# Kernel optimization log

Hardware: AMD Instinct MI355X
Metric: run time of the kernel (lower is better)

## Reference

```python
import jax, jax.numpy as jnp
import numpy as np

B, N, E, DJ, DE = 1024, 400, 128, 128, 128  # batch, nodes, edges, joint dim, edge dim (E must equal DJ and DE for BatchNorm1d on 3D input)
BN_EPS = 1e-5


def setup_inputs() -> dict:
    key = jax.random.key(0)
    ks = jax.random.split(key, 8)
    gout = jax.random.normal(ks[0], (B, N, DJ), dtype=jnp.float32)
    eout = jax.random.normal(ks[1], (B, E, DE), dtype=jnp.float32)
    start_shift = jax.random.uniform(ks[2], (B, E, N), dtype=jnp.float32)
    end_shift = jax.random.uniform(ks[3], (B, E, N), dtype=jnp.float32)
    # Linear params: nn.init.normal_(std=0.001), bias 0
    W1 = 0.001 * jax.random.normal(ks[4], (DJ, 2 * DJ), dtype=jnp.float32)
    b1 = jnp.zeros((DJ,), dtype=jnp.float32)
    W2 = 0.001 * jax.random.normal(ks[5], (DE, DJ), dtype=jnp.float32)
    b2 = jnp.zeros((DE,), dtype=jnp.float32)
    # BatchNorm affine params: weight=1, bias=0
    g1 = jnp.ones((DJ,), dtype=jnp.float32)
    beta1 = jnp.zeros((DJ,), dtype=jnp.float32)
    g2 = jnp.ones((DE,), dtype=jnp.float32)
    beta2 = jnp.zeros((DE,), dtype=jnp.float32)
    return {"gout": gout, "eout": eout, "start_shift": start_shift, "end_shift": end_shift,
            "W1": W1, "b1": b1, "W2": W2, "b2": b2,
            "g1": g1, "beta1": beta1, "g2": g2, "beta2": beta2}


def batchnorm1d(x, gamma, beta):
    # PyTorch BatchNorm1d on 3D input: channels at dim 1, biased variance over dims (0, 2)
    mean = jnp.mean(x, axis=(0, 2), keepdims=True)
    var = jnp.mean(jnp.square(x - mean), axis=(0, 2), keepdims=True)
    xhat = (x - mean) * jax.lax.rsqrt(var + BN_EPS)
    return xhat * gamma[None, :, None] + beta[None, :, None]


def reference(gout, eout, start_shift, end_shift, W1, b1, W2, b2, g1, beta1, g2, beta2):
    # node -> edge gather via dense shift matmuls: [B,E,N] @ [B,N,DJ] -> [B,E,DJ]
    start_nodes = jnp.matmul(start_shift, gout)
    end_nodes = jnp.matmul(end_shift, gout)
    x = jnp.concatenate([start_nodes, end_nodes], axis=2)  # [B, E, 2*DJ]
    h = jnp.einsum('bef,df->bed', x, W1) + b1  # Linear(2*DJ -> DJ)
    h = jax.nn.relu(batchnorm1d(h, g1, beta1))
    h = jnp.einsum('bed,od->beo', h, W2) + b2  # Linear(DJ -> DE)
    res = batchnorm1d(h, g2, beta2)
    return jax.nn.relu(eout + res)
```

## Files before the change

kernel.cpp:

```cpp
#include <hip/hip_runtime.h>
#include <stdint.h>

#define BB 1024
#define NN 400
#define EE 128
#define DD 128
#define NSLOT 64

typedef float f32x4 __attribute__((ext_vector_type(4)));
typedef float f32x2 __attribute__((ext_vector_type(2)));
typedef short bf16x8 __attribute__((ext_vector_type(8)));
typedef short bf16x4 __attribute__((ext_vector_type(4)));

__device__ __forceinline__ short f2bf(float f) {
    uint32_t u = __builtin_bit_cast(uint32_t, f);
    u += 0x7fffu + ((u >> 16) & 1u);
    return (short)(u >> 16);
}

__device__ __forceinline__ float bf2f(short s) {
    return __builtin_bit_cast(float, (uint32_t)((uint16_t)s) << 16);
}

__device__ __forceinline__ bf16x8 cvt8(const f32x4 a, const f32x4 b) {
    bf16x8 r;
    r[0] = f2bf(a[0]); r[1] = f2bf(a[1]); r[2] = f2bf(a[2]); r[3] = f2bf(a[3]);
    r[4] = f2bf(b[0]); r[5] = f2bf(b[1]); r[6] = f2bf(b[2]); r[7] = f2bf(b[3]);
    return r;
}

__global__ __launch_bounds__(256, 4)
void k1_gemm(const float* __restrict__ gout, const float* __restrict__ ss,
             const float* __restrict__ es, const float* __restrict__ W1,
             const float* __restrict__ b1, unsigned short* __restrict__ h,
             float* __restrict__ stats1)
{
    __shared__ short lds[16384];
    short* As = lds;
    short* Gs = lds + 5120;
    short* Ps = lds;

    const int bid = blockIdx.x;
    const int b   = bid >> 1;
    const int e0  = (bid & 1) * 64;
    const int t   = threadIdx.x;
    const int w   = t >> 6;
    const int l15 = t & 15;
    const int l4  = (t >> 4) & 3;

    f32x4 acc[2][8];
#pragma unroll
    for (int i = 0; i < 2; ++i)
#pragma unroll
        for (int j = 0; j < 8; ++j) acc[i][j] = f32x4{0.f, 0.f, 0.f, 0.f};

    f32x4 ar[4];
    const int arow = t >> 3;
    const int acol = (t & 7) * 4;
    f32x2 g0[4], g1[4];
    const int gx = t & 31;
    const int gk = (t >> 5) * 2;

    auto load_a = [&](int k0) {
#pragma unroll
        for (int p = 0; p < 4; ++p) {
            int row = arow + 32 * p;
            int col = k0 + acol;
            const float* src = (row < 64)
                ? ss + (size_t)(b * EE + e0 + row) * NN + col
                : es + (size_t)(b * EE + e0 + row - 64) * NN + col;
            ar[p] = (col < NN) ? *(const f32x4*)src : f32x4{0.f, 0.f, 0.f, 0.f};
        }
    };
    auto load_g = [&](int k0) {
#pragma unroll
        for (int p = 0; p < 4; ++p) {
            int d0 = 2 * gx + 64 * (p & 1);
            int k  = k0 + gk + 16 * (p >> 1);
            const float* base = gout + (size_t)b * NN * DD + (size_t)k * DD + d0;
            g0[p] = (k < NN)     ? *(const f32x2*)base        : f32x2{0.f, 0.f};
            g1[p] = (k + 1 < NN) ? *(const f32x2*)(base + DD) : f32x2{0.f, 0.f};
        }
    };
    auto store_a = [&]() {
#pragma unroll
        for (int p = 0; p < 4; ++p) {
            int row = arow + 32 * p;
            bf16x4 v;
            v[0] = f2bf(ar[p][0]); v[1] = f2bf(ar[p][1]);
            v[2] = f2bf(ar[p][2]); v[3] = f2bf(ar[p][3]);
            *(bf16x4*)&As[row * 40 + acol] = v;
        }
    };
    auto store_g = [&]() {
#pragma unroll
        for (int p = 0; p < 4; ++p) {
            int d0 = 2 * gx + 64 * (p & 1);
            int kp = gk + 16 * (p >> 1);
            uint32_t lo = (uint32_t)(uint16_t)f2bf(g0[p][0]) |
                          ((uint32_t)(uint16_t)f2bf(g1[p][0]) << 16);
            uint32_t hi = (uint32_t)(uint16_t)f2bf(g0[p][1]) |
                          ((uint32_t)(uint16_t)f2bf(g1[p][1]) << 16);
            int c  = (kp >> 3) ^ ((d0 >> 2) & 3);
            int a0 = d0 * 40 + (c << 3) + (kp & 7);
            *(uint32_t*)&Gs[a0]      = lo;
            *(uint32_t*)&Gs[a0 + 40] = hi;
        }
    };

    load_a(0); load_g(0);
    const int NK = (NN + 31) / 32;
    for (int step = 0; step < NK; ++step) {
        store_a(); store_g();
        __syncthreads();
        if (step + 1 < NK) { load_a((step + 1) * 32); load_g((step + 1) * 32); }
        bf16x8 af[2];
#pragma unroll
        for (int rf = 0; rf < 2; ++rf) {
            int row = w * 32 + rf * 16 + l15;
            af[rf] = *(const bf16x8*)&As[row * 40 + l4 * 8];
        }
#pragma unroll
        for (int cf = 0; cf < 8; ++cf) {
            int col = cf * 16 + l15;
            int cc  = l4 ^ ((col >> 2) & 3);
            bf16x8 bfr = *(const bf16x8*)&Gs[col * 40 + cc * 8];
            acc[0][cf] = __builtin_amdgcn_mfma_f32_16x16x32_bf16(af[0], bfr, acc[0][cf], 0, 0, 0);
            acc[1][cf] = __builtin_amdgcn_mfma_f32_16x16x32_bf16(af[1], bfr, acc[1][cf], 0, 0, 0);
        }
        __syncthreads();
    }

#pragma unroll
    for (int rf = 0; rf < 2; ++rf)
#pragma unroll
        for (int cf = 0; cf < 8; ++cf)
#pragma unroll
            for (int r = 0; r < 4; ++r) {
                int row = w * 32 + rf * 16 + l4 * 4 + r;
                int col = cf * 16 + l15;
                int off = row * 128 + (((col >> 3) ^ (row & 7)) * 8) + (col & 7);
                Ps[off] = f2bf(acc[rf][cf][r]);
            }
    __syncthreads();

    f32x4 hacc[4][2];
#pragma unroll
    for (int i = 0; i < 4; ++i) {
        hacc[i][0] = f32x4{0.f, 0.f, 0.f, 0.f};
        hacc[i][1] = f32x4{0.f, 0.f, 0.f, 0.f};
    }
#pragma unroll
    for (int kf = 0; kf < 8; ++kf) {
        const int k0   = kf * 32;
        const int roff = (kf >= 4) ? 64 : 0;
        const int cb   = ((k0 & 127) >> 3) + l4;
        bf16x8 af[4];
#pragma unroll
        for (int rf = 0; rf < 4; ++rf) {
            int row = roff + rf * 16 + l15;
            af[rf] = *(const bf16x8*)&Ps[row * 128 + ((cb ^ (row & 7)) * 8)];
        }
#pragma unroll
        for (int cf = 0; cf < 2; ++cf) {
            int j = w * 32 + cf * 16 + l15;
            const float* wp = W1 + (size_t)j * 256 + k0 + l4 * 8;
            bf16x8 bfr = cvt8(*(const f32x4*)wp, *(const f32x4*)(wp + 4));
#pragma unroll
            for (int rf = 0; rf < 4; ++rf)
                hacc[rf][cf] = __builtin_amdgcn_mfma_f32_16x16x32_bf16(af[rf], bfr, hacc[rf][cf], 0, 0, 0);
        }
    }
    __syncthreads();

    float* red = (float*)lds;
    const float bj0 = b1[w * 32 + l15];
    const float bj1 = b1[w * 32 + 16 + l15];
    const int j0 = w * 32 + l15;
#pragma unroll
    for (int rf = 0; rf < 4; ++rf) {
        f32x4 v0 = hacc[rf][0] + bj0;
        f32x4 v1 = hacc[rf][1] + bj1;
        int elb = rf * 16 + l4 * 4;
#pragma unroll
        for (int r = 0; r < 4; ++r) {
            unsigned short* hp = h + (size_t)(b * EE + e0 + elb + r) * DD;
            hp[j0]      = (unsigned short)f2bf(v0[r]);
            hp[j0 + 16] = (unsigned short)f2bf(v1[r]);
            float s = v0[r] + v1[r];
            float q = v0[r] * v0[r] + v1[r] * v1[r];
            s += __shfl_xor(s, 1); s += __shfl_xor(s, 2); s += __shfl_xor(s, 4); s += __shfl_xor(s, 8);
            q += __shfl_xor(q, 1); q += __shfl_xor(q, 2); q += __shfl_xor(q, 4); q += __shfl_xor(q, 8);
            if (l15 == 0) {
                red[(elb + r) * 4 + w]       = s;
                red[256 + (elb + r) * 4 + w] = q;
            }
        }
    }
    __syncthreads();
    if (t < 64) {
        float s = red[t * 4] + red[t * 4 + 1] + red[t * 4 + 2] + red[t * 4 + 3];
        float q = red[256 + t * 4] + red[256 + t * 4 + 1] + red[256 + t * 4 + 2] + red[256 + t * 4 + 3];
        int slot = bid & (NSLOT - 1);
        atomicAdd(&stats1[slot * 256 + e0 + t], s);
        atomicAdd(&stats1[slot * 256 + 128 + e0 + t], q);
    }
}

__global__ __launch_bounds__(256, 4)
void k3_gemm(const unsigned short* __restrict__ h, const float* __restrict__ W2,
             const float* __restrict__ b2, const float* __restrict__ g1,
             const float* __restrict__ bt1, float* __restrict__ out,
             const float* __restrict__ stats1, float* __restrict__ stats2)
{
    __shared__ short Xs[128 * 128];
    __shared__ float sc[128];
    __shared__ float sh[128];
    const int b   = blockIdx.x;
    const int t   = threadIdx.x;
    const int w   = t >> 6;
    const int l15 = t & 15;
    const int l4  = (t >> 4) & 3;

    if (t < 128) {
        float sm = 0.f, sq = 0.f;
#pragma unroll 8
        for (int sl = 0; sl < NSLOT; ++sl) {
            sm += stats1[sl * 256 + t];
            sq += stats1[sl * 256 + 128 + t];
        }
        const float inv_n = 1.0f / (1024.0f * 128.0f);
        float m    = sm * inv_n;
        float var  = sq * inv_n - m * m;
        float rstd = rsqrtf(var + 1e-5f);
        float s    = rstd * g1[t];
        sc[t] = s;
        sh[t] = bt1[t] - m * s;
    }
    __syncthreads();

    {
        const int c8 = t & 15;
        const int eb = t >> 4;
#pragma unroll
        for (int p = 0; p < 8; ++p) {
            int e = eb + 16 * p;
            bf16x8 v8 = *(const bf16x8*)&h[((size_t)b * EE + e) * DD + c8 * 8];
            float s = sc[e], s0 = sh[e];
            bf16x8 o;
#pragma unroll
            for (int i = 0; i < 8; ++i)
                o[i] = f2bf(fmaxf(fmaf(bf2f(v8[i]), s, s0), 0.0f));
            *(bf16x8*)&Xs[e * 128 + ((c8 ^ (e & 7)) << 3)] = o;
        }
    }
    __syncthreads();

    f32x4 acc[8][2];
#pragma unroll
    for (int i = 0; i < 8; ++i) {
        acc[i][0] = f32x4{0.f, 0.f, 0.f, 0.f};
        acc[i][1] = f32x4{0.f, 0.f, 0.f, 0.f};
    }
#pragma unroll
    for (int kf = 0; kf < 4; ++kf) {
        const int k0 = kf * 32;
        const int cb = (k0 >> 3) + l4;
        bf16x8 af[8];
#pragma unroll
        for (int rf = 0; rf < 8; ++rf) {
            int row = rf * 16 + l15;
            af[rf] = *(const bf16x8*)&Xs[row * 128 + ((cb ^ (row & 7)) * 8)];
        }
#pragma unroll
        for (int cf = 0; cf < 2; ++cf) {
            int j = w * 32 + cf * 16 + l15;
            const float* wp = W2 + (size_t)j * 128 + k0 + l4 * 8;
            bf16x8 bfr = cvt8(*(const f32x4*)wp, *(const f32x4*)(wp + 4));
#pragma unroll
            for (int rf = 0; rf < 8; ++rf)
                acc[rf][cf] = __builtin_amdgcn_mfma_f32_16x16x32_bf16(af[rf], bfr, acc[rf][cf], 0, 0, 0);
        }
    }

    __syncthreads();
    float* red = (float*)Xs;
    const float bj0 = b2[w * 32 + l15];
    const float bj1 = b2[w * 32 + 16 + l15];
    const int j0 = w * 32 + l15;
#pragma unroll
    for (int rf = 0; rf < 8; ++rf) {
        f32x4 v0 = acc[rf][0] + bj0;
        f32x4 v1 = acc[rf][1] + bj1;
        int elb = rf * 16 + l4 * 4;
#pragma unroll
        for (int r = 0; r < 4; ++r) {
            float* op = out + (size_t)(b * EE + elb + r) * DD;
            op[j0]      = v0[r];
            op[j0 + 16] = v1[r];
            float s = v0[r] + v1[r];
            float q = v0[r] * v0[r] + v1[r] * v1[r];
            s += __shfl_xor(s, 1); s += __shfl_xor(s, 2); s += __shfl_xor(s, 4); s += __shfl_xor(s, 8);
            q += __shfl_xor(q, 1); q += __shfl_xor(q, 2); q += __shfl_xor(q, 4); q += __shfl_xor(q, 8);
            if (l15 == 0) {
                red[(elb + r) * 4 + w]       = s;
                red[512 + (elb + r) * 4 + w] = q;
            }
        }
    }
    __syncthreads();
    if (t < 128) {
        float s = red[t * 4] + red[t * 4 + 1] + red[t * 4 + 2] + red[t * 4 + 3];
        float q = red[512 + t * 4] + red[512 + t * 4 + 1] + red[512 + t * 4 + 2] + red[512 + t * 4 + 3];
        int slot = b & (NSLOT - 1);
        atomicAdd(&stats2[slot * 256 + t], s);
        atomicAdd(&stats2[slot * 256 + 128 + t], q);
    }
}

__global__ __launch_bounds__(256)
void k5_final(const float* __restrict__ eout, const float* __restrict__ g2,
              const float* __restrict__ bt2, float* __restrict__ io,
              const float* __restrict__ stats2)
{
    __shared__ float sc[128];
    __shared__ float sh[128];
    const int t = threadIdx.x;
    if (t < 128) {
        float sm = 0.f, sq = 0.f;
#pragma unroll 8
        for (int sl = 0; sl < NSLOT; ++sl) {
            sm += stats2[sl * 256 + t];
            sq += stats2[sl * 256 + 128 + t];
        }
        const float inv_n = 1.0f / (1024.0f * 128.0f);
        float m    = sm * inv_n;
        float var  = sq * inv_n - m * m;
        float rstd = rsqrtf(var + 1e-5f);
        float s    = rstd * g2[t];
        sc[t] = s;
        sh[t] = bt2[t] - m * s;
    }
    __syncthreads();

    const int total4 = BB * EE * DD / 4;
    for (int i4 = blockIdx.x * blockDim.x + t; i4 < total4; i4 += gridDim.x * blockDim.x) {
        int e = (i4 >> 5) & 127;
        f32x4 v = *(f32x4*)(io + (size_t)i4 * 4);
        f32x4 u = *(const f32x4*)(eout + (size_t)i4 * 4);
        float s = sc[e], s0 = sh[e];
        f32x4 o;
#pragma unroll
        for (int i = 0; i < 4; ++i)
            o[i] = fmaxf(u[i] + fmaf(v[i], s, s0), 0.0f);
        *(f32x4*)(io + (size_t)i4 * 4) = o;
    }
}

extern "C" void kernel_launch(void* const* d_in, const int* in_sizes, int n_in,
                              void* d_out, int out_size, void* d_ws, size_t ws_size,
                              hipStream_t stream)
{
    const float* gout  = (const float*)d_in[0];
    const float* eout  = (const float*)d_in[1];
    const float* ss    = (const float*)d_in[2];
    const float* es    = (const float*)d_in[3];
    const float* W1    = (const float*)d_in[4];
    const float* b1    = (const float*)d_in[5];
    const float* W2    = (const float*)d_in[6];
    const float* b2    = (const float*)d_in[7];
    const float* g1    = (const float*)d_in[8];
    const float* bt1   = (const float*)d_in[9];
    const float* g2    = (const float*)d_in[10];
    const float* bt2   = (const float*)d_in[11];

    float* stats1 = (float*)d_ws;
    float* stats2 = stats1 + NSLOT * 256;
    unsigned short* h = (unsigned short*)(stats2 + NSLOT * 256);
    float* out    = (float*)d_out;

    hipMemsetAsync((void*)stats1, 0, 2 * NSLOT * 256 * sizeof(float), stream);
    k1_gemm<<<dim3(BB * 2), dim3(256), 0, stream>>>(gout, ss, es, W1, b1, h, stats1);
    k3_gemm<<<dim3(BB), dim3(256), 0, stream>>>(h, W2, b2, g1, bt1, out, stats1, stats2);
    k5_final<<<dim3(2048), dim3(256), 0, stream>>>(eout, g2, bt2, out, stats2);
}
```

Baseline: 258.0 us.

## Restructure k1 to one 1024-thread block per batch with full gout staged in LDS

The first GEMM kernel now runs one 1024-thread block per batch instead of two 256-thread blocks. The whole transposed gout tile is converted to bf16 once into LDS, so it is no longer loaded twice per batch. Shift-matrix rows stream straight from global memory into MFMA A fragments, with register prefetch in place of LDS staging and per-step barriers. W1 is staged in LDS as bf16 for the second GEMM instead of being re-read from global by every wave. The cost is about 133KB of LDS per block, which allows only one block per CU, and the shift-matrix global loads are less coalesced.

```diff
diff --git a/kernel.cpp b/kernel.cpp
--- a/kernel.cpp
+++ b/kernel.cpp
@@ -6,9 +6,10 @@
 #define EE 128
 #define DD 128
 #define NSLOT 64
+#define GTS 424
+#define NKP 212
 
 typedef float f32x4 __attribute__((ext_vector_type(4)));
-typedef float f32x2 __attribute__((ext_vector_type(2)));
 typedef short bf16x8 __attribute__((ext_vector_type(8)));
 typedef short bf16x4 __attribute__((ext_vector_type(4)));
 
@@ -29,181 +30,145 @@
     return r;
 }
 
-__global__ __launch_bounds__(256, 4)
+__global__ __launch_bounds__(1024, 1)
 void k1_gemm(const float* __restrict__ gout, const float* __restrict__ ss,
              const float* __restrict__ es, const float* __restrict__ W1,
              const float* __restrict__ b1, unsigned short* __restrict__ h,
              float* __restrict__ stats1)
 {
-    __shared__ short lds[16384];
-    short* As = lds;
-    short* Gs = lds + 5120;
-    short* Ps = lds;
-
-    const int bid = blockIdx.x;
-    const int b   = bid >> 1;
-    const int e0  = (bid & 1) * 64;
+    __shared__ short lds[66560];
+    short* GT  = lds;
+    short* Ps  = lds;
+    short* W1s = lds + 32768;
+
+    const int b   = blockIdx.x;
     const int t   = threadIdx.x;
     const int w   = t >> 6;
-    const int l15 = t & 15;
-    const int l4  = (t >> 4) & 3;
-
-    f32x4 acc[2][8];
-#pragma unroll
-    for (int i = 0; i < 2; ++i)
-#pragma unroll
-        for (int j = 0; j < 8; ++j) acc[i][j] = f32x4{0.f, 0.f, 0.f, 0.f};
-
-    f32x4 ar[4];
-    const int arow = t >> 3;
-    const int acol = (t & 7) * 4;
-    f32x2 g0[4], g1[4];
-    const int gx = t & 31;
-    const int gk = (t >> 5) * 2;
-
-    auto load_a = [&](int k0) {
-#pragma unroll
-        for (int p = 0; p < 4; ++p) {
-            int row = arow + 32 * p;
-            int col = k0 + acol;
-            const float* src = (row < 64)
-                ? ss + (size_t)(b * EE + e0 + row) * NN + col
-                : es + (size_t)(b * EE + e0 + row - 64) * NN + col;
-            ar[p] = (col < NN) ? *(const f32x4*)src : f32x4{0.f, 0.f, 0.f, 0.f};
-        }
+    const int l   = t & 63;
+    const int l15 = l & 15;
+    const int l4  = l >> 4;
+
+    {
+        const int d   = t & 127;
+        const int kpb = t >> 7;
+        const float* gb = gout + (size_t)b * NN * DD + d;
+        for (int kp = kpb; kp < NKP; kp += 8) {
+            int k = 2 * kp;
+            float v0 = 0.f, v1 = 0.f;
+            if (k < NN) { v0 = gb[(size_t)k * DD]; v1 = gb[(size_t)(k + 1) * DD]; }
+            uint32_t pk = (uint32_t)(uint16_t)f2bf(v0) |
+                          ((uint32_t)(uint16_t)f2bf(v1) << 16);
+            *(uint32_t*)&GT[d * GTS + 2 * kp] = pk;
+        }
+    }
+    __syncthreads();
+
+    const int arow = (w & 7) * 16 + l15;
+    const float* abase = ((w < 8) ? ss : es) + ((size_t)b * EE + arow) * NN;
+
+    f32x4 acc[8];
+#pragma unroll
+    for (int cf = 0; cf < 8; ++cf) acc[cf] = f32x4{0.f, 0.f, 0.f, 0.f};
+
+    auto ld_a = [&](int k0) -> bf16x8 {
+        int kk = k0 + l4 * 8;
+        f32x4 x0{0.f, 0.f, 0.f, 0.f}, x1{0.f, 0.f, 0.f, 0.f};
+        if (kk < NN) { x0 = *(const f32x4*)(abase + kk); x1 = *(const f32x4*)(abase + kk + 4); }
+        return cvt8(x0, x1);
     };
-    auto load_g = [&](int k0) {
-#pragma unroll
-        for (int p = 0; p < 4; ++p) {
-            int d0 = 2 * gx + 64 * (p & 1);
-            int k  = k0 + gk + 16 * (p >> 1);
-            const float* base = gout + (size_t)b * NN * DD + (size_t)k * DD + d0;
-            g0[p] = (k < NN)     ? *(const f32x2*)base        : f32x2{0.f, 0.f};
-            g1[p] = (k + 1 < NN) ? *(const f32x2*)(base + DD) : f32x2{0.f, 0.f};
-        }
-    };
-    auto store_a = [&]() {
-#pragma unroll
-        for (int p = 0; p < 4; ++p) {
-            int row = arow + 32 * p;
-            bf16x4 v;
-            v[0] = f2bf(ar[p][0]); v[1] = f2bf(ar[p][1]);
-            v[2] = f2bf(ar[p][2]); v[3] = f2bf(ar[p][3]);
-            *(bf16x4*)&As[row * 40 + acol] = v;
-        }
-    };
-    auto store_g = [&]() {
-#pragma unroll
-        for (int p = 0; p < 4; ++p) {
-            int d0 = 2 * gx + 64 * (p & 1);
-            int kp = gk + 16 * (p >> 1);
-            uint32_t lo = (uint32_t)(uint16_t)f2bf(g0[p][0]) |
-                          ((uint32_t)(uint16_t)f2bf(g1[p][0]) << 16);
-            uint32_t hi = (uint32_t)(uint16_t)f2bf(g0[p][1]) |
-                          ((uint32_t)(uint16_t)f2bf(g1[p][1]) << 16);
-            int c  = (kp >> 3) ^ ((d0 >> 2) & 3);
-            int a0 = d0 * 40 + (c << 3) + (kp & 7);
-            *(uint32_t*)&Gs[a0]      = lo;
-            *(uint32_t*)&Gs[a0 + 40] = hi;
-        }
-    };
-
-    load_a(0); load_g(0);
-    const int NK = (NN + 31) / 32;
-    for (int step = 0; step < NK; ++step) {
-        store_a(); store_g();
-        __syncthreads();
-        if (step + 1 < NK) { load_a((step + 1) * 32); load_g((step + 1) * 32); }
-        bf16x8 af[2];
-#pragma unroll
-        for (int rf = 0; rf < 2; ++rf) {
-            int row = w * 32 + rf * 16 + l15;
-            af[rf] = *(const bf16x8*)&As[row * 40 + l4 * 8];
-        }
+
+    bf16x8 a_cur = ld_a(0);
+    const int NK = 13;
+    for (int s = 0; s < NK; ++s) {
+        bf16x8 a_nxt = a_cur;
+        if (s + 1 < NK) a_nxt = ld_a((s + 1) * 32);
+        const int k0 = s * 32;
 #pragma unroll
         for (int cf = 0; cf < 8; ++cf) {
+            bf16x8 gf = *(const bf16x8*)&GT[(cf * 16 + l15) * GTS + k0 + l4 * 8];
+            acc[cf] = __builtin_amdgcn_mfma_f32_16x16x32_bf16(a_cur, gf, acc[cf], 0, 0, 0);
+        }
+        a_cur = a_nxt;
+    }
+    __syncthreads();
+
+#pragma unroll
+    for (int cf = 0; cf < 8; ++cf)
+#pragma unroll
+        for (int r = 0; r < 4; ++r) {
+            int row = w * 16 + l4 * 4 + r;
             int col = cf * 16 + l15;
-            int cc  = l4 ^ ((col >> 2) & 3);
-            bf16x8 bfr = *(const bf16x8*)&Gs[col * 40 + cc * 8];
-            acc[0][cf] = __builtin_amdgcn_mfma_f32_16x16x32_bf16(af[0], bfr, acc[0][cf], 0, 0, 0);
-            acc[1][cf] = __builtin_amdgcn_mfma_f32_16x16x32_bf16(af[1], bfr, acc[1][cf], 0, 0, 0);
-        }
-        __syncthreads();
-    }
-
-#pragma unroll
-    for (int rf = 0; rf < 2; ++rf)
-#pragma unroll
-        for (int cf = 0; cf < 8; ++cf)
-#pragma unroll
-            for (int r = 0; r < 4; ++r) {
-                int row = w * 32 + rf * 16 + l4 * 4 + r;
-                int col = cf * 16 + l15;
-                int off = row * 128 + (((col >> 3) ^ (row & 7)) * 8) + (col & 7);
-                Ps[off] = f2bf(acc[rf][cf][r]);
-            }
-    __syncthreads();
-
-    f32x4 hacc[4][2];
-#pragma unroll
-    for (int i = 0; i < 4; ++i) {
-        hacc[i][0] = f32x4{0.f, 0.f, 0.f, 0.f};
-        hacc[i][1] = f32x4{0.f, 0.f, 0.f, 0.f};
-    }
+            Ps[row * 128 + (((col >> 3) ^ (row & 7)) << 3) + (col & 7)] = f2bf(acc[cf][r]);
+        }
+    {
+        const int j  = t >> 3;
+        const int kc = t & 7;
+        const float* wp = W1 + (size_t)j * 256 + kc * 32;
+        short* dst = &W1s[j * 264 + kc * 32];
+#pragma unroll
+        for (int i = 0; i < 4; ++i) {
+            f32x4 x0 = *(const f32x4*)(wp + i * 8);
+            f32x4 x1 = *(const f32x4*)(wp + i * 8 + 4);
+            *(bf16x8*)(dst + i * 8) = cvt8(x0, x1);
+        }
+    }
+    __syncthreads();
+
+    const int mt = w >> 1;
+    const int jh = w & 1;
+    f32x4 acc2[4];
+#pragma unroll
+    for (int cf = 0; cf < 4; ++cf) acc2[cf] = f32x4{0.f, 0.f, 0.f, 0.f};
+
 #pragma unroll
     for (int kf = 0; kf < 8; ++kf) {
-        const int k0   = kf * 32;
-        const int roff = (kf >= 4) ? 64 : 0;
-        const int cb   = ((k0 & 127) >> 3) + l4;
-        bf16x8 af[4];
-#pragma unroll
-        for (int rf = 0; rf < 4; ++rf) {
-            int row = roff + rf * 16 + l15;
-            af[rf] = *(const bf16x8*)&Ps[row * 128 + ((cb ^ (row & 7)) * 8)];
-        }
-#pragma unroll
-        for (int cf = 0; cf < 2; ++cf) {
-            int j = w * 32 + cf * 16 + l15;
-            const float* wp = W1 + (size_t)j * 256 + k0 + l4 * 8;
-            bf16x8 bfr = cvt8(*(const f32x4*)wp, *(const f32x4*)(wp + 4));
-#pragma unroll
-            for (int rf = 0; rf < 4; ++rf)
-                hacc[rf][cf] = __builtin_amdgcn_mfma_f32_16x16x32_bf16(af[rf], bfr, hacc[rf][cf], 0, 0, 0);
+        int roff = (kf >= 4) ? 128 : 0;
+        int kcol = (kf & 3) * 32 + l4 * 8;
+        int row  = roff + mt * 16 + l15;
+        int cb   = kcol >> 3;
+        bf16x8 xf = *(const bf16x8*)&Ps[row * 128 + ((cb ^ (row & 7)) << 3)];
+#pragma unroll
+        for (int cf = 0; cf < 4; ++cf) {
+            int j = jh * 64 + cf * 16 + l15;
+            bf16x8 wf = *(const bf16x8*)&W1s[j * 264 + kf * 32 + l4 * 8];
+            acc2[cf] = __builtin_amdgcn_mfma_f32_16x16x32_bf16(xf, wf, acc2[cf], 0, 0, 0);
         }
     }
     __syncthreads();
 
     float* red = (float*)lds;
-    const float bj0 = b1[w * 32 + l15];
-    const float bj1 = b1[w * 32 + 16 + l15];
-    const int j0 = w * 32 + l15;
-#pragma unroll
-    for (int rf = 0; rf < 4; ++rf) {
-        f32x4 v0 = hacc[rf][0] + bj0;
-        f32x4 v1 = hacc[rf][1] + bj1;
-        int elb = rf * 16 + l4 * 4;
+    float s_r[4] = {0.f, 0.f, 0.f, 0.f};
+    float q_r[4] = {0.f, 0.f, 0.f, 0.f};
+#pragma unroll
+    for (int cf = 0; cf < 4; ++cf) {
+        float bv = b1[jh * 64 + cf * 16 + l15];
+        f32x4 v = acc2[cf] + bv;
 #pragma unroll
         for (int r = 0; r < 4; ++r) {
-            unsigned short* hp = h + (size_t)(b * EE + e0 + elb + r) * DD;
-            hp[j0]      = (unsigned short)f2bf(v0[r]);
-            hp[j0 + 16] = (unsigned short)f2bf(v1[r]);
-            float s = v0[r] + v1[r];
-            float q = v0[r] * v0[r] + v1[r] * v1[r];
-            s += __shfl_xor(s, 1); s += __shfl_xor(s, 2); s += __shfl_xor(s, 4); s += __shfl_xor(s, 8);
-            q += __shfl_xor(q, 1); q += __shfl_xor(q, 2); q += __shfl_xor(q, 4); q += __shfl_xor(q, 8);
-            if (l15 == 0) {
-                red[(elb + r) * 4 + w]       = s;
-                red[256 + (elb + r) * 4 + w] = q;
-            }
-        }
-    }
-    __syncthreads();
-    if (t < 64) {
-        float s = red[t * 4] + red[t * 4 + 1] + red[t * 4 + 2] + red[t * 4 + 3];
-        float q = red[256 + t * 4] + red[256 + t * 4 + 1] + red[256 + t * 4 + 2] + red[256 + t * 4 + 3];
-        int slot = bid & (NSLOT - 1);
-        atomicAdd(&stats1[slot * 256 + e0 + t], s);
-        atomicAdd(&stats1[slot * 256 + 128 + e0 + t], q);
+            int e = mt * 16 + l4 * 4 + r;
+            h[((size_t)b * EE + e) * DD + jh * 64 + cf * 16 + l15] = (unsigned short)f2bf(v[r]);
+            s_r[r] += v[r];
+            q_r[r] += v[r] * v[r];
+        }
+    }
+#pragma unroll
+    for (int r = 0; r < 4; ++r) {
+        float s = s_r[r], q = q_r[r];
+        s += __shfl_xor(s, 1); s += __shfl_xor(s, 2); s += __shfl_xor(s, 4); s += __shfl_xor(s, 8);
+        q += __shfl_xor(q, 1); q += __shfl_xor(q, 2); q += __shfl_xor(q, 4); q += __shfl_xor(q, 8);
+        if (l15 == 0) {
+            int e = mt * 16 + l4 * 4 + r;
+            red[((e << 1) | jh)]       = s;
+            red[256 + ((e << 1) | jh)] = q;
+        }
+    }
+    __syncthreads();
+    if (t < 128) {
+        float s = red[2 * t] + red[2 * t + 1];
+        float q = red[256 + 2 * t] + red[256 + 2 * t + 1];
+        int slot = b & (NSLOT - 1);
+        atomicAdd(&stats1[slot * 256 + t], s);
+        atomicAdd(&stats1[slot * 256 + 128 + t], q);
     }
 }
 
@@ -380,7 +345,7 @@
     float* out    = (float*)d_out;
 
     hipMemsetAsync((void*)stats1, 0, 2 * NSLOT * 256 * sizeof(float), stream);
-    k1_gemm<<<dim3(BB * 2), dim3(256), 0, stream>>>(gout, ss, es, W1, b1, h, stats1);
+    k1_gemm<<<dim3(BB), dim3(1024), 0, stream>>>(gout, ss, es, W1, b1, h, stats1);
     k3_gemm<<<dim3(BB), dim3(256), 0, stream>>>(h, W2, b2, g1, bt1, out, stats1, stats2);
     k5_final<<<dim3(2048), dim3(256), 0, stream>>>(eout, g2, bt2, out, stats2);
 }
```

New measurement: 263.6 us. 2.2% more time.
